# Performance work log

Measured on AMD Instinct MI355X. Metric: run time of the kernel, lower is better.

The kernel has to match this reference:

```python
import jax, jax.numpy as jnp
import numpy as np

THRESHOLD = 0.35      # overlap_thresh
NEGPOS_RATIO = 7
VAR0, VAR1 = 0.1, 0.2  # self.variance


def make_priors():
    # Standard RetinaFace 640x640 anchor grid -> 16800 priors (cx, cy, w, h)
    img = 640
    steps = [8, 16, 32]
    min_sizes = [[16, 32], [64, 128], [256, 512]]
    out = []
    for step, ms in zip(steps, min_sizes):
        f = img // step
        ii, jj = np.meshgrid(np.arange(f), np.arange(f), indexing="ij")
        cx = ((jj + 0.5) * step / img).ravel().astype(np.float32)
        cy = ((ii + 0.5) * step / img).ravel().astype(np.float32)
        for m in ms:
            s = np.full_like(cx, m / img)
            out.append(np.stack([cx, cy, s, s], axis=-1))
    return jnp.asarray(np.concatenate(out, axis=0), dtype=jnp.float32)


def jaccard(a, b):
    # a: [O,4] point-form gt boxes, b: [P,4] point-form priors -> IoU [O,P]
    lt = jnp.maximum(a[:, None, :2], b[None, :, :2])
    rb = jnp.minimum(a[:, None, 2:], b[None, :, 2:])
    wh = jnp.clip(rb - lt, 0.0)
    inter = wh[..., 0] * wh[..., 1]
    area_a = ((a[:, 2] - a[:, 0]) * (a[:, 3] - a[:, 1]))[:, None]
    area_b = ((b[:, 2] - b[:, 0]) * (b[:, 3] - b[:, 1]))[None, :]
    return inter / (area_a + area_b - inter)


def setup_inputs() -> dict:
    key = jax.random.key(0)
    ks = jax.random.split(key, 7)
    B, P, O = 64, 16800, 64
    loc_data = jax.random.normal(ks[0], (B, P, 4), jnp.float32)
    conf_data = jax.random.normal(ks[1], (B, P, 2), jnp.float32)
    landm_data = jax.random.normal(ks[2], (B, P, 10), jnp.float32)
    priors = make_priors()
    # targets: [B, O, 15] = [xmin ymin xmax ymax | 10 landmark coords | label]
    c = jax.random.uniform(ks[3], (B, O, 2), minval=0.15, maxval=0.85)
    wh = jax.random.uniform(ks[4], (B, O, 2), minval=0.05, maxval=0.3)
    boxes = jnp.concatenate([jnp.clip(c - wh / 2, 1e-3, 0.999),
                             jnp.clip(c + wh / 2, 1e-3, 0.999)], axis=-1)
    landms = jax.random.uniform(ks[5], (B, O, 10))
    lab = jnp.where(jax.random.uniform(ks[6], (B, O, 1)) < 0.8, 1.0, -1.0)
    targets = jnp.concatenate([boxes, landms, lab], axis=-1).astype(jnp.float32)
    return {"loc_data": loc_data, "conf_data": conf_data,
            "landm_data": landm_data, "priors": priors, "targets": targets}


def _smooth_l1(x):
    ax = jnp.abs(x)
    return jnp.where(ax < 1.0, 0.5 * ax * ax, ax - 0.5)


def reference(loc_data, conf_data, landm_data, priors, targets):
    B, P, C = conf_data.shape
    O = targets.shape[1]
    priors_pf = jnp.concatenate([priors[:, :2] - priors[:, 2:] * 0.5,
                                 priors[:, :2] + priors[:, 2:] * 0.5], axis=1)

    def match_one(t):
        truths = t[:, :4]
        landms = t[:, 4:14]
        labels = t[:, 14].astype(jnp.int32)
        ov = jaccard(truths, priors_pf)               # [O,P]
        bp_ov = ov.max(axis=1)                         # best prior per truth
        bp_idx = jnp.argmax(ov, axis=1)
        valid = bp_ov >= 0.2                           # RetinaFace gt filter
        bt_ov = ov.max(axis=0)                         # best truth per prior
        bt_idx = jnp.argmax(ov, axis=0)
        # index_fill_(best_prior_idx, 2) for valid gts, ensure best prior kept
        bt_ov = bt_ov.at[bp_idx].set(jnp.where(valid, 2.0, bt_ov[bp_idx]))
        bt_idx = bt_idx.at[bp_idx].set(jnp.arange(O))
        matched = truths[bt_idx]                       # [P,4] point form
        conf = labels[bt_idx]
        conf = jnp.where(bt_ov < THRESHOLD, 0, conf)
        # encode loc target
        g_cxcy = ((matched[:, :2] + matched[:, 2:]) * 0.5 - priors[:, :2]) / (VAR0 * priors[:, 2:])
        g_wh = jnp.log((matched[:, 2:] - matched[:, :2]) / priors[:, 2:]) / VAR1
        loc = jnp.concatenate([g_cxcy, g_wh], axis=1)
        # encode landmark target (5 points)
        ml = landms[bt_idx].reshape(P, 5, 2)
        lm = ((ml - priors[:, None, :2]) / (VAR0 * priors[:, None, 2:])).reshape(P, 10)
        any_valid = jnp.any(valid)                     # early-return branch of match()
        return (jnp.where(any_valid, loc, 0.0),
                jnp.where(any_valid, conf, 0),
                jnp.where(any_valid, lm, 0.0))

    loc_t, conf_t, landm_t = jax.vmap(match_one)(targets)
    loc_t = jax.lax.stop_gradient(loc_t)       # targets built from .data in torch
    landm_t = jax.lax.stop_gradient(landm_t)

    # landmark loss over conf_t > 0
    pos1 = conf_t > 0
    N1 = jnp.maximum(pos1.sum().astype(jnp.float32), 1.0)
    loss_landm = jnp.sum(jnp.where(pos1[..., None], _smooth_l1(landm_data - landm_t), 0.0))

    # localization loss over conf_t != 0 (labels -1 and 1 both positive)
    pos = conf_t != 0
    conf_t1 = jnp.where(pos, 1, conf_t)        # conf_t[pos] = 1 -> values in {0,1}
    loss_l = jnp.sum(jnp.where(pos[..., None], _smooth_l1(loc_data - loc_t), 0.0))

    # hard negative mining
    lse = jax.nn.logsumexp(conf_data, axis=2)                       # [B,P]
    picked = jnp.take_along_axis(conf_data, conf_t1[..., None], axis=2)[..., 0]
    ce_all = lse - picked                                            # per-anchor CE
    rank_score = jnp.where(pos, 0.0, ce_all)
    loss_idx = jnp.argsort(-rank_score, axis=1)
    idx_rank = jnp.argsort(loss_idx, axis=1)
    num_pos = pos.sum(axis=1, keepdims=True)
    num_neg = jnp.minimum(NEGPOS_RATIO * num_pos, P - 1)
    neg = idx_rank < num_neg
    union = pos | neg
    loss_c = jnp.sum(jnp.where(union, ce_all, 0.0))

    N = jnp.maximum(num_pos.sum().astype(jnp.float32), 1.0)
    return loss_l / N, loss_c / N, loss_landm / N1
```

## Files before the change

kernel.cpp:

```cpp
#include <hip/hip_runtime.h>
#include <math.h>

#define B 64
#define P 16800
#define O 64
#define THRESH 0.35f
#define VALID_T 0.2f
#define HB 2048
#define HSHIFT 21
#define AREA_M 0.34f
#define MULT 2
#define CHB (MULT * 256)
#define NB2 ((P + CHB - 1) / CHB)
#define KD1B (B * NB2)
#define KB2B (B * O / 4)

__device__ __forceinline__ float smooth_l1(float x) {
    float ax = fabsf(x);
    return ax < 1.f ? 0.5f * ax * ax : ax - 0.5f;
}
__device__ __forceinline__ float lse2(float c0, float c1) {
    float m = fmaxf(c0, c1);
    return m + __logf(__expf(c0 - m) + __expf(c1 - m));
}
__device__ __forceinline__ void iou_upd(float4 t, float area_a,
                                        float px1, float py1, float px2, float py2,
                                        float area_b,
                                        float& bnum, float& bden, int& bio, int o) {
    float w = fmaxf(fminf(t.z, px2) - fmaxf(t.x, px1), 0.f);
    float h = fmaxf(fminf(t.w, py2) - fmaxf(t.y, py1), 0.f);
    float inter = w * h;
    float den = area_a + area_b - inter;
    if (inter * bden > bnum * den) { bnum = inter; bden = den; bio = o; }
}
__device__ __forceinline__ float wave_sum(float v) {
#pragma unroll
    for (int s = 32; s > 0; s >>= 1) v += __shfl_down(v, s, 64);
    return v;
}
__device__ __forceinline__ int wave_sum_i(int v) {
#pragma unroll
    for (int s = 32; s > 0; s >>= 1) v += __shfl_down(v, s, 64);
    return v;
}
__device__ __forceinline__ float wave_min(float v) {
#pragma unroll
    for (int s = 32; s > 0; s >>= 1) v = fminf(v, __shfl_xor(v, s, 64));
    return v;
}
__device__ __forceinline__ float wave_max(float v) {
#pragma unroll
    for (int s = 32; s > 0; s >>= 1) v = fmaxf(v, __shfl_xor(v, s, 64));
    return v;
}
__device__ __forceinline__ int wave_sufscan(int v, int lane) {
#pragma unroll
    for (int s = 1; s < 64; s <<= 1) {
        int o = __shfl_down(v, s, 64);
        if (lane + s < 64) v += o;
    }
    return v;
}

__global__ void __launch_bounds__(256) kMain(
        const float* __restrict__ loc_data, const float* __restrict__ conf_data,
        const float* __restrict__ landm_data, const float* __restrict__ priors,
        const float* __restrict__ targets,
        float* __restrict__ rank,
        int* __restrict__ num_pos, float* __restrict__ pos_ce,
        float* __restrict__ gsum, int* __restrict__ np1_tot,
        unsigned long long* __restrict__ bp_final) {
    if (blockIdx.x >= KD1B) {
        int pair = (blockIdx.x - KD1B) * 4 + (threadIdx.x >> 6);
        int lane = threadIdx.x & 63;
        int o = pair & (O - 1);
        int b = pair >> 6;
        const float* tt = &targets[(b * O + o) * 15];
        float tx1 = tt[0], ty1 = tt[1], tx2 = tt[2], ty2 = tt[3];
        float area_a = (tx2 - tx1) * (ty2 - ty1);
        float4 tb = make_float4(tx1, ty1, tx2, ty2);
        float bn = 0.f, bd = 1.f;
        unsigned bp = 0u;
        const int fs[6]   = {80, 80, 40, 40, 20, 20};
        const int ms[6]   = {16, 32, 64, 128, 256, 512};
        const int base[6] = {0, 6400, 12800, 14400, 16000, 16400};
#pragma unroll
        for (int c = 0; c < 6; ++c) {
            int f = fs[c];
            float inv = (float)f;
            float h = (float)ms[c] * (0.5f / 640.f);
            int j0 = (int)floorf((tx1 - h) * inv - 0.5f) - 1; if (j0 < 0) j0 = 0;
            int j1 = (int)ceilf((tx2 + h) * inv - 0.5f) + 1;  if (j1 > f - 1) j1 = f - 1;
            int i0 = (int)floorf((ty1 - h) * inv - 0.5f) - 1; if (i0 < 0) i0 = 0;
            int i1 = (int)ceilf((ty2 + h) * inv - 0.5f) + 1;  if (i1 > f - 1) i1 = f - 1;
            if (j1 < j0 || i1 < i0) continue;
            int nj = j1 - j0 + 1;
            int n = (i1 - i0 + 1) * nj;
            float rcp_nj = 1.0f / (float)nj;
            for (int idx = lane; idx < n; idx += 64) {
                int ii = (int)((float)idx * rcp_nj);
                int jj = idx - ii * nj;
                if (jj < 0) { ii--; jj += nj; } else if (jj >= nj) { ii++; jj -= nj; }
                int p = base[c] + (i0 + ii) * f + (j0 + jj);
                float4 q = ((const float4*)priors)[p];
                float px1 = q.x - q.z * 0.5f, py1 = q.y - q.w * 0.5f;
                float px2 = q.x + q.z * 0.5f, py2 = q.y + q.w * 0.5f;
                float areab = (px2 - px1) * (py2 - py1);
                float w = fmaxf(fminf(tb.z, px2) - fmaxf(tb.x, px1), 0.f);
                float hh = fmaxf(fminf(tb.w, py2) - fmaxf(tb.y, py1), 0.f);
                float inter = w * hh;
                float den = area_a + areab - inter;
                float l = bn * den, r = inter * bd;
                if (r > l) { bn = inter; bd = den; bp = (unsigned)p; }
            }
        }
#pragma unroll
        for (int s = 32; s > 0; s >>= 1) {
            float no = __shfl_xor(bn, s, 64), dd = __shfl_xor(bd, s, 64);
            unsigned po = __shfl_xor(bp, s, 64);
            float l = bn * dd, r = no * bd;
            bool take = (r > l) || (r == l && po < bp);
            if (take) { bn = no; bd = dd; bp = po; }
        }
        if (lane == 0) {
            float iou = bn / bd;
            bp_final[b * O + o] = ((unsigned long long)__float_as_uint(iou) << 32)
                                | (unsigned)(0xFFFFFFFFu - bp);
        }
        return;
    }
    int blk = blockIdx.x % NB2;
    int b = blockIdx.x / NB2;
    int p0 = blk * CHB;
    __shared__ float4 t4[O];
    __shared__ float ta[O], lab[O];
    __shared__ float lm[O][10];
    __shared__ float4 wbb[4];
    __shared__ float2 wab[4];
    __shared__ int alist[O];
    __shared__ int s_cnt;
    __shared__ float wredf[3][4];
    __shared__ int wredi[2][4];
    int tid = threadIdx.x;
    if (tid < O) {
        const float* t = &targets[(b * O + tid) * 15];
        float a0 = t[0], a1 = t[1], a2 = t[2], a3 = t[3];
        t4[tid] = make_float4(a0, a1, a2, a3);
        ta[tid] = (a2 - a0) * (a3 - a1);
        lab[tid] = t[14];
    }
    for (int i = tid; i < O * 10; i += 256)
        lm[i / 10][i % 10] = targets[b * O * 15 + (i / 10) * 15 + 4 + (i % 10)];
    float px1[MULT], py1[MULT], px2[MULT], py2[MULT], areab[MULT];
    float4 pr4[MULT];
    float bnum[MULT], bden[MULT]; int bi[MULT]; bool act[MULT];
    float bx1 = 1e30f, by1 = 1e30f, bx2 = -1e30f, by2 = -1e30f;
    float amn = 1e30f, amx = -1e30f;
#pragma unroll
    for (int mi = 0; mi < MULT; ++mi) {
        int p = p0 + mi * 256 + tid;
        act[mi] = (p < P);
        int pc = act[mi] ? p : (P - 1);
        float4 q = ((const float4*)priors)[pc];
        pr4[mi] = q;
        px1[mi] = q.x - q.z * 0.5f; py1[mi] = q.y - q.w * 0.5f;
        px2[mi] = q.x + q.z * 0.5f; py2[mi] = q.y + q.w * 0.5f;
        areab[mi] = (px2[mi] - px1[mi]) * (py2[mi] - py1[mi]);
        bx1 = fminf(bx1, px1[mi]); by1 = fminf(by1, py1[mi]);
        bx2 = fmaxf(bx2, px2[mi]); by2 = fmaxf(by2, py2[mi]);
        amn = fminf(amn, areab[mi]); amx = fmaxf(amx, areab[mi]);
        bnum[mi] = 0.f; bden[mi] = 1.f; bi[mi] = 0;
    }
    bx1 = wave_min(bx1); by1 = wave_min(by1);
    bx2 = wave_max(bx2); by2 = wave_max(by2);
    amn = wave_min(amn); amx = wave_max(amx);
    int wid = tid >> 6, lid = tid & 63;
    if (lid == 0) { wbb[wid] = make_float4(bx1, by1, bx2, by2); wab[wid] = make_float2(amn, amx); }
    __syncthreads();
    if (tid < 64) {
        float ux1 = fminf(fminf(wbb[0].x, wbb[1].x), fminf(wbb[2].x, wbb[3].x));
        float uy1 = fminf(fminf(wbb[0].y, wbb[1].y), fminf(wbb[2].y, wbb[3].y));
        float ux2 = fmaxf(fmaxf(wbb[0].z, wbb[1].z), fmaxf(wbb[2].z, wbb[3].z));
        float uy2 = fmaxf(fmaxf(wbb[0].w, wbb[1].w), fmaxf(wbb[2].w, wbb[3].w));
        float bmn = fminf(fminf(wab[0].x, wab[1].x), fminf(wab[2].x, wab[3].x));
        float bmx = fmaxf(fmaxf(wab[0].y, wab[1].y), fmaxf(wab[2].y, wab[3].y));
        float4 t = t4[tid];
        float Aa = ta[tid];
        bool pass = (fminf(t.z, ux2) - fmaxf(t.x, ux1) > 0.f) &&
                    (fminf(t.w, uy2) - fmaxf(t.y, uy1) > 0.f) &&
                    (Aa >= AREA_M * bmn) && (bmx >= AREA_M * Aa);
        unsigned long long mask = __ballot(pass);
        if (tid == 0) s_cnt = __popcll(mask);
        if (pass) {
            int pos = __popcll(mask & ((1ull << tid) - 1ull));
            alist[pos] = tid;
        }
    }
    __syncthreads();
    int cnt = s_cnt;
    for (int li = 0; li < cnt; ++li) {
        int o = alist[li];
        float4 t = t4[o];
        float w0 = fminf(t.z, bx2) - fmaxf(t.x, bx1);
        float h0 = fminf(t.w, by2) - fmaxf(t.y, by1);
        if (w0 <= 0.f || h0 <= 0.f) continue;
        float Aa = ta[o];
#pragma unroll
        for (int mi = 0; mi < MULT; ++mi) {
            float Ap = areab[mi];
            if (Aa >= AREA_M * Ap && Ap >= AREA_M * Aa)
                iou_upd(t, Aa, px1[mi], py1[mi], px2[mi], py2[mi], Ap,
                        bnum[mi], bden[mi], bi[mi], o);
        }
    }
    float ll = 0.f, llm = 0.f, cep = 0.f;
    int cp = 0, cp1 = 0;
#pragma unroll
    for (int mi = 0; mi < MULT; ++mi) {
        if (!act[mi]) continue;
        int p = p0 + mi * 256 + tid;
        float best = bnum[mi] / bden[mi];
        int conf = (best >= THRESH) ? (int)lab[bi[mi]] : 0;
        float2 c01 = ((const float2*)conf_data)[b * P + p];
        float c0 = c01.x, c1 = c01.y;
        float lse = lse2(c0, c1);
        bool pos = conf != 0;
        float ce = lse - (pos ? c1 : c0);
        float rv = pos ? 0.f : ce;
        rank[(size_t)b * P + p] = rv;
        if (pos) {
            cp++; cep += ce;
            int ti = bi[mi];
            float cx = pr4[mi].x, cy = pr4[mi].y, sw = pr4[mi].z, sh = pr4[mi].w;
            float4 t = t4[ti];
            float gx = ((t.x + t.z) * 0.5f - cx) / (0.1f * sw);
            float gy = ((t.y + t.w) * 0.5f - cy) / (0.1f * sh);
            float gw = logf((t.z - t.x) / sw) / 0.2f;
            float gh = logf((t.w - t.y) / sh) / 0.2f;
            const float* ld = &loc_data[(size_t)(b * P + p) * 4];
            ll += smooth_l1(ld[0] - gx) + smooth_l1(ld[1] - gy) +
                  smooth_l1(ld[2] - gw) + smooth_l1(ld[3] - gh);
            if (conf > 0) {
                cp1++;
                const float* lmd = &landm_data[(size_t)(b * P + p) * 10];
                for (int k5 = 0; k5 < 5; ++k5) {
                    float lx = (lm[ti][k5 * 2 + 0] - cx) / (0.1f * sw);
                    float ly = (lm[ti][k5 * 2 + 1] - cy) / (0.1f * sh);
                    llm += smooth_l1(lmd[k5 * 2 + 0] - lx) + smooth_l1(lmd[k5 * 2 + 1] - ly);
                }
            }
        }
    }
    float s_ll = wave_sum(ll), s_llm = wave_sum(llm), s_cep = wave_sum(cep);
    int s_cp = wave_sum_i(cp), s_cp1 = wave_sum_i(cp1);
    if (lid == 0) {
        wredf[0][wid] = s_ll; wredf[1][wid] = s_llm; wredf[2][wid] = s_cep;
        wredi[0][wid] = s_cp; wredi[1][wid] = s_cp1;
    }
    __syncthreads();
    if (tid == 0) {
        float ll_t = wredf[0][0] + wredf[0][1] + wredf[0][2] + wredf[0][3];
        float llm_t = wredf[1][0] + wredf[1][1] + wredf[1][2] + wredf[1][3];
        float cep_t = wredf[2][0] + wredf[2][1] + wredf[2][2] + wredf[2][3];
        int cp_t = wredi[0][0] + wredi[0][1] + wredi[0][2] + wredi[0][3];
        int cp1_t = wredi[1][0] + wredi[1][1] + wredi[1][2] + wredi[1][3];
        if (ll_t != 0.f)  atomicAdd(&gsum[0], ll_t);
        if (llm_t != 0.f) atomicAdd(&gsum[1], llm_t);
        if (cep_t != 0.f) atomicAdd(&pos_ce[b], cep_t);
        if (cp_t)  atomicAdd(&num_pos[b], cp_t);
        if (cp1_t) atomicAdd(np1_tot, cp1_t);
    }
}

__global__ void __launch_bounds__(1024) kTail(
        const float* __restrict__ priors, const float* __restrict__ targets,
        const float* __restrict__ loc_data, const float* __restrict__ conf_data,
        const float* __restrict__ landm_data,
        const unsigned long long* __restrict__ bp_final,
        const float* __restrict__ rank,
        const int* __restrict__ num_pos, const float* __restrict__ pos_ce,
        float* __restrict__ gsum, int* __restrict__ np1_tot, int* __restrict__ np_tot,
        float* __restrict__ lossc_tot, int* __restrict__ done,
        float* __restrict__ out) {
    __shared__ __align__(16) unsigned lrow[P];
    __shared__ float4 t4[O];
    __shared__ float ta[O], lab[O];
    __shared__ int sp[O];
    __shared__ int lh[HB];
    __shared__ int chunkSum[256];
    __shared__ int suf[257];
    __shared__ int waveTot[4];
    __shared__ int hist2[256];
    __shared__ int s_np, s_bin0, s_kk0, s_bin, s_kk;
    __shared__ float wredf[16];
    __shared__ int wredi[16];
    __shared__ float s_sumgt;

    int b = blockIdx.x;
    int tid = threadIdx.x;
    const float* r = rank + (size_t)b * P;
    const float4* r4 = (const float4*)r;
    for (int i = tid; i < P / 4; i += 1024) {
        float4 q = r4[i];
        ((uint4*)lrow)[i] = make_uint4(__float_as_uint(q.x), __float_as_uint(q.y),
                                       __float_as_uint(q.z), __float_as_uint(q.w));
    }
    for (int i = tid; i < HB; i += 1024) lh[i] = 0;
    int p = 0, v = 0;
    if (tid < O) {
        const float* tt = &targets[(b * O + tid) * 15];
        float4 tj = make_float4(tt[0], tt[1], tt[2], tt[3]);
        t4[tid] = tj;
        ta[tid] = (tj.z - tj.x) * (tj.w - tj.y);
        lab[tid] = tt[14];
        unsigned long long kpk = bp_final[b * O + tid];
        p = (int)(0xFFFFFFFFu - (unsigned)(kpk & 0xFFFFFFFFu));
        float iou = __uint_as_float((unsigned)(kpk >> 32));
        v = (iou >= VALID_T) ? 1 : 0;
        sp[tid] = p;
    }
    __syncthreads();
    for (int i = tid; i < P; i += 1024) atomicAdd(&lh[lrow[i] >> HSHIFT], 1);
    __syncthreads();
    int dnp = 0, dn1 = 0;
    float dll = 0.f, dllm = 0.f, dce = 0.f;
    if (tid < O) {
        int j = tid;
        bool winner = true;
        for (int jj = j + 1; jj < O; ++jj)
            if (sp[jj] == p) { winner = false; break; }
        if (winner) {
            float4 q = ((const float4*)priors)[p];
            float px1 = q.x - q.z * 0.5f, py1 = q.y - q.w * 0.5f;
            float px2 = q.x + q.z * 0.5f, py2 = q.y + q.w * 0.5f;
            float areab = (px2 - px1) * (py2 - py1);
            float bnum = 0.f, bden = 1.f; int bi = 0;
            for (int o = 0; o < O; ++o) {
                float Aa = ta[o];
                if (Aa >= AREA_M * areab && areab >= AREA_M * Aa)
                    iou_upd(t4[o], Aa, px1, py1, px2, py2, areab, bnum, bden, bi, o);
            }
            float best = bnum / bden;
            float ov_new = v ? 2.0f : best;
            int conf_old = (best >= THRESH) ? (int)lab[bi] : 0;
            int conf_new = (ov_new >= THRESH) ? (int)lab[j] : 0;
            float2 c01 = ((const float2*)conf_data)[b * P + p];
            float c0 = c01.x, c1 = c01.y;
            float lse = lse2(c0, c1);
            bool po = conf_old != 0, pn = conf_new != 0;
            float ceo = lse - (po ? c1 : c0), cen = lse - (pn ? c1 : c0);
            float rvo = po ? 0.f : ceo, rvn = pn ? 0.f : cen;
            if (__float_as_uint(rvo) != __float_as_uint(rvn)) {
                lrow[p] = __float_as_uint(rvn);
                int bo = __float_as_uint(rvo) >> HSHIFT, bn = __float_as_uint(rvn) >> HSHIFT;
                if (bo != bn) { atomicAdd(&lh[bn], 1); atomicAdd(&lh[bo], -1); }
            }
            const float* ld = &loc_data[(size_t)(b * P + p) * 4];
            auto enc_ll = [&](int ti) -> float {
                float4 t = t4[ti];
                float gx = ((t.x + t.z) * 0.5f - q.x) / (0.1f * q.z);
                float gy = ((t.y + t.w) * 0.5f - q.y) / (0.1f * q.w);
                float gw = logf((t.z - t.x) / q.z) / 0.2f;
                float gh = logf((t.w - t.y) / q.w) / 0.2f;
                return smooth_l1(ld[0] - gx) + smooth_l1(ld[1] - gy) +
                       smooth_l1(ld[2] - gw) + smooth_l1(ld[3] - gh);
            };
            if (po) dll -= enc_ll(bi);
            if (pn) dll += enc_ll(j);
            dce = (pn ? cen : 0.f) - (po ? ceo : 0.f);
            dnp = (int)pn - (int)po;
            const float* lmd = &landm_data[(size_t)(b * P + p) * 10];
            auto enc_lm = [&](int ti) -> float {
                const float* lmt = &targets[(b * O + ti) * 15 + 4];
                float sum = 0.f;
                for (int k5 = 0; k5 < 5; ++k5) {
                    float lx = (lmt[k5 * 2 + 0] - q.x) / (0.1f * q.z);
                    float ly = (lmt[k5 * 2 + 1] - q.y) / (0.1f * q.w);
                    sum += smooth_l1(lmd[k5 * 2 + 0] - lx) + smooth_l1(lmd[k5 * 2 + 1] - ly);
                }
                return sum;
            };
            if (conf_old > 0) dllm -= enc_lm(bi);
            if (conf_new > 0) dllm += enc_lm(j);
            dn1 = (int)(conf_new > 0) - (int)(conf_old > 0);
        }
    }
    float pce_reg = 0.f;
    if (tid < 64) {
        float r_ll = wave_sum(dll), r_lm = wave_sum(dllm), r_ce = wave_sum(dce);
        int r_np = wave_sum_i(dnp), r_n1 = wave_sum_i(dn1);
        if (tid == 0) {
            if (r_ll != 0.f) atomicAdd(&gsum[0], r_ll);
            if (r_lm != 0.f) atomicAdd(&gsum[1], r_lm);
            pce_reg = pos_ce[b] + r_ce;
            int np = num_pos[b] + r_np;
            s_np = np;
            atomicAdd(np_tot, np);
            if (r_n1) atomicAdd(np1_tot, r_n1);
        }
    }
    __syncthreads();
    int k = s_np * 7;
    if (k > P - 1) k = P - 1;
    if (tid < 256) {
        int cs = 0;
#pragma unroll
        for (int i = 0; i < HB / 256; ++i) cs += lh[tid * (HB / 256) + i];
        chunkSum[tid] = cs;
    }
    if (tid == 0) { s_bin0 = (k <= 0) ? -1 : 0; s_kk0 = (k <= 0) ? 0 : k; }
    __syncthreads();
    {
        int lane = tid & 63;
        int vv = (tid < 256) ? chunkSum[tid] : 0;
        vv = wave_sufscan(vv, lane);
        if (tid < 256 && lane == 0) waveTot[tid >> 6] = vv;
        __syncthreads();
        if (tid < 256) {
            int after = 0;
            for (int g = (tid >> 6) + 1; g < 4; ++g) after += waveTot[g];
            suf[tid] = vv + after;
            if (tid == 0) suf[256] = 0;
        }
        __syncthreads();
        if (k > 0 && tid < 256) {
            if (suf[tid] >= k && suf[tid + 1] < k) {
                int cum = suf[tid + 1];
                for (int i = HB / 256 - 1; i >= 0; --i) {
                    int hv = lh[tid * (HB / 256) + i];
                    if (cum + hv >= k) { s_bin0 = tid * (HB / 256) + i; s_kk0 = k - cum; break; }
                    cum += hv;
                }
            }
        }
    }
    __syncthreads();
    int bin = s_bin0;
    int kk0 = s_kk0;
    float topk_b = 0.f;
    if (bin >= 0) {
        unsigned lo_bound = ((unsigned)(bin + 1)) << HSHIFT;
        float sumgt = 0.f;
        for (int pp = tid; pp < P; pp += 1024) {
            unsigned u = lrow[pp];
            if (u >= lo_bound) sumgt += __uint_as_float(u);
        }
        float sg = wave_sum(sumgt);
        if ((tid & 63) == 0) wredf[tid >> 6] = sg;
        __syncthreads();
        if (tid == 0) {
            float t = 0.f;
            for (int i = 0; i < 16; ++i) t += wredf[i];
            s_sumgt = t;
        }
        unsigned pref = ((unsigned)bin) << HSHIFT;
        unsigned resolved = 0xFFFFFFFFu << HSHIFT;
        int kk = kk0;
        const int shifts[3] = {13, 5, 0};
        const int nbins[3] = {256, 256, 32};
        for (int pass = 0; pass < 3; ++pass) {
            int sh = shifts[pass], nb = nbins[pass];
            if (tid < nb) hist2[tid] = 0;
            __syncthreads();
            for (int i = tid; i < P / 4; i += 1024) {
                uint4 u4 = ((const uint4*)lrow)[i];
                if ((u4.x & resolved) == pref) atomicAdd(&hist2[(u4.x >> sh) & (nb - 1)], 1);
                if ((u4.y & resolved) == pref) atomicAdd(&hist2[(u4.y >> sh) & (nb - 1)], 1);
                if ((u4.z & resolved) == pref) atomicAdd(&hist2[(u4.z >> sh) & (nb - 1)], 1);
                if ((u4.w & resolved) == pref) atomicAdd(&hist2[(u4.w >> sh) & (nb - 1)], 1);
            }
            __syncthreads();
            int lane = tid & 63;
            int vv = (tid < nb) ? hist2[tid] : 0;
            vv = wave_sufscan(vv, lane);
            if (tid < nb && lane == 0) waveTot[tid >> 6] = vv;
            __syncthreads();
            int ng = (nb + 63) >> 6;
            if (tid < nb) {
                int after = 0;
                for (int g = (tid >> 6) + 1; g < ng; ++g) after += waveTot[g];
                suf[tid] = vv + after;
                if (tid == 0) suf[nb] = 0;
            }
            __syncthreads();
            if (tid < nb) {
                if (suf[tid] >= kk && suf[tid + 1] < kk) { s_bin = tid; s_kk = kk - suf[tid + 1]; }
            }
            __syncthreads();
            pref |= ((unsigned)s_bin) << sh;
            resolved |= (unsigned)(nb - 1) << sh;
            kk = s_kk;
            __syncthreads();
        }
        float tv = __uint_as_float(pref);
        float sumS = 0.f; int cntS = 0;
        for (int pp = tid; pp < P; pp += 1024) {
            unsigned u = lrow[pp];
            if ((u >> HSHIFT) == (unsigned)bin) {
                float val = __uint_as_float(u);
                if (val > tv) { sumS += val; cntS++; }
            }
        }
        float s2 = wave_sum(sumS); int c2 = wave_sum_i(cntS);
        if ((tid & 63) == 0) { wredf[tid >> 6] = s2; wredi[tid >> 6] = c2; }
        __syncthreads();
        if (tid == 0) {
            float st = 0.f; int ct = 0;
            for (int i = 0; i < 16; ++i) { st += wredf[i]; ct += wredi[i]; }
            topk_b = s_sumgt + st + (float)(kk0 - ct) * tv;
        }
    }
    if (tid == 0) {
        atomicAdd(lossc_tot, pce_reg + topk_b);
        __threadfence();
        int old = atomicAdd(done, 1);
        if (old == B - 1) {
            float g0 = atomicAdd(&gsum[0], 0.f);
            float g1 = atomicAdd(&gsum[1], 0.f);
            float lc = atomicAdd(lossc_tot, 0.f);
            int np = atomicAdd(np_tot, 0);
            int n1 = atomicAdd(np1_tot, 0);
            float N = fmaxf((float)np, 1.f);
            float N1 = fmaxf((float)n1, 1.f);
            out[0] = g0 / N;
            out[1] = lc / N;
            out[2] = g1 / N1;
        }
    }
}

extern "C" void kernel_launch(void* const* d_in, const int* in_sizes, int n_in,
                              void* d_out, int out_size, void* d_ws, size_t ws_size,
                              hipStream_t stream) {
    const float* loc_data   = (const float*)d_in[0];
    const float* conf_data  = (const float*)d_in[1];
    const float* landm_data = (const float*)d_in[2];
    const float* priors     = (const float*)d_in[3];
    const float* targets    = (const float*)d_in[4];
    float* out = (float*)d_out;

    char* ws = (char*)d_ws;
    size_t off = 0;
    auto alloc = [&](size_t bytes) -> void* {
        void* pp = ws + off;
        off += (bytes + 255) & ~(size_t)255;
        return pp;
    };
    float* rank     = (float*)alloc((size_t)B * P * 4);
    unsigned long long* bp_final = (unsigned long long*)alloc((size_t)B * O * 8);
    size_t acc_bytes = (size_t)(2 * B * 4 + 64);
    char* acc = (char*)alloc(acc_bytes);
    int*   num_pos      = (int*)acc;
    float* pos_ce       = (float*)(acc + B * 4);
    float* gsum         = (float*)(acc + 2 * B * 4);
    int*   np1_tot      = (int*)(acc + 2 * B * 4 + 8);
    int*   np_tot       = (int*)(acc + 2 * B * 4 + 12);
    float* lossc_tot    = (float*)(acc + 2 * B * 4 + 16);
    int*   done         = (int*)(acc + 2 * B * 4 + 20);

    hipMemsetAsync(acc, 0, acc_bytes, stream);
    kMain<<<dim3(KD1B + KB2B), dim3(256), 0, stream>>>(loc_data, conf_data, landm_data,
                                                       priors, targets, rank,
                                                       num_pos, pos_ce, gsum, np1_tot,
                                                       bp_final);
    kTail<<<dim3(B), dim3(1024), 0, stream>>>(priors, targets, loc_data, conf_data,
                                              landm_data, bp_final, rank,
                                              num_pos, pos_ce, gsum, np1_tot, np_tot,
                                              lossc_tot, done, out);
}
```

Measured before the change: 166.8 us.

## Compact radix-select candidates into shared memory and fuse histogram with row load

The per-batch top-k radix select now builds the first histogram while copying the rank row into shared memory. During the tail-sum pass it compacts values from the boundary bin into a shared candidate list (capped at CCAP) and builds the second-level histogram in the same pass, so later refinement passes scan only the candidates instead of the full row. The first kernel doubles MULT to 4 priors per thread and stages the raw targets with one float4 copy into shared memory. These changes add shared memory use and a fallback path when the candidate list overflows.

Result: slower. 170.9 us (+2.4%).

```diff
diff --git a/kernel.cpp b/kernel.cpp
--- a/kernel.cpp
+++ b/kernel.cpp
@@ -9,7 +9,8 @@
 #define HB 2048
 #define HSHIFT 21
 #define AREA_M 0.34f
-#define MULT 2
+#define CCAP 4096
+#define MULT 4
 #define CHB (MULT * 256)
 #define NB2 ((P + CHB - 1) / CHB)
 #define KD1B (B * NB2)
@@ -132,9 +133,9 @@
     int blk = blockIdx.x % NB2;
     int b = blockIdx.x / NB2;
     int p0 = blk * CHB;
+    __shared__ float traw[O * 15];
     __shared__ float4 t4[O];
     __shared__ float ta[O], lab[O];
-    __shared__ float lm[O][10];
     __shared__ float4 wbb[4];
     __shared__ float2 wab[4];
     __shared__ int alist[O];
@@ -142,15 +143,8 @@
     __shared__ float wredf[3][4];
     __shared__ int wredi[2][4];
     int tid = threadIdx.x;
-    if (tid < O) {
-        const float* t = &targets[(b * O + tid) * 15];
-        float a0 = t[0], a1 = t[1], a2 = t[2], a3 = t[3];
-        t4[tid] = make_float4(a0, a1, a2, a3);
-        ta[tid] = (a2 - a0) * (a3 - a1);
-        lab[tid] = t[14];
-    }
-    for (int i = tid; i < O * 10; i += 256)
-        lm[i / 10][i % 10] = targets[b * O * 15 + (i / 10) * 15 + 4 + (i % 10)];
+    if (tid < O * 15 / 4)
+        ((float4*)traw)[tid] = ((const float4*)(targets + (size_t)b * O * 15))[tid];
     float px1[MULT], py1[MULT], px2[MULT], py2[MULT], areab[MULT];
     float4 pr4[MULT];
     float bnum[MULT], bden[MULT]; int bi[MULT]; bool act[MULT];
@@ -178,14 +172,19 @@
     if (lid == 0) { wbb[wid] = make_float4(bx1, by1, bx2, by2); wab[wid] = make_float2(amn, amx); }
     __syncthreads();
     if (tid < 64) {
+        const float* tr = &traw[tid * 15];
+        float a0 = tr[0], a1 = tr[1], a2 = tr[2], a3 = tr[3];
+        float4 t = make_float4(a0, a1, a2, a3);
+        t4[tid] = t;
+        float Aa = (a2 - a0) * (a3 - a1);
+        ta[tid] = Aa;
+        lab[tid] = tr[14];
         float ux1 = fminf(fminf(wbb[0].x, wbb[1].x), fminf(wbb[2].x, wbb[3].x));
         float uy1 = fminf(fminf(wbb[0].y, wbb[1].y), fminf(wbb[2].y, wbb[3].y));
         float ux2 = fmaxf(fmaxf(wbb[0].z, wbb[1].z), fmaxf(wbb[2].z, wbb[3].z));
         float uy2 = fmaxf(fmaxf(wbb[0].w, wbb[1].w), fmaxf(wbb[2].w, wbb[3].w));
         float bmn = fminf(fminf(wab[0].x, wab[1].x), fminf(wab[2].x, wab[3].x));
         float bmx = fmaxf(fmaxf(wab[0].y, wab[1].y), fmaxf(wab[2].y, wab[3].y));
-        float4 t = t4[tid];
-        float Aa = ta[tid];
         bool pass = (fminf(t.z, ux2) - fmaxf(t.x, ux1) > 0.f) &&
                     (fminf(t.w, uy2) - fmaxf(t.y, uy1) > 0.f) &&
                     (Aa >= AREA_M * bmn) && (bmx >= AREA_M * Aa);
@@ -243,9 +242,10 @@
             if (conf > 0) {
                 cp1++;
                 const float* lmd = &landm_data[(size_t)(b * P + p) * 10];
+                const float* lmt = &traw[ti * 15 + 4];
                 for (int k5 = 0; k5 < 5; ++k5) {
-                    float lx = (lm[ti][k5 * 2 + 0] - cx) / (0.1f * sw);
-                    float ly = (lm[ti][k5 * 2 + 1] - cy) / (0.1f * sh);
+                    float lx = (lmt[k5 * 2 + 0] - cx) / (0.1f * sw);
+                    float ly = (lmt[k5 * 2 + 1] - cy) / (0.1f * sh);
                     llm += smooth_l1(lmd[k5 * 2 + 0] - lx) + smooth_l1(lmd[k5 * 2 + 1] - ly);
                 }
             }
@@ -291,7 +291,8 @@
     __shared__ int suf[257];
     __shared__ int waveTot[4];
     __shared__ int hist2[256];
-    __shared__ int s_np, s_bin0, s_kk0, s_bin, s_kk;
+    __shared__ unsigned lcand[CCAP];
+    __shared__ int s_np, s_bin0, s_kk0, s_bin, s_kk, s_cnt;
     __shared__ float wredf[16];
     __shared__ int wredi[16];
     __shared__ float s_sumgt;
@@ -299,13 +300,8 @@
     int b = blockIdx.x;
     int tid = threadIdx.x;
     const float* r = rank + (size_t)b * P;
-    const float4* r4 = (const float4*)r;
-    for (int i = tid; i < P / 4; i += 1024) {
-        float4 q = r4[i];
-        ((uint4*)lrow)[i] = make_uint4(__float_as_uint(q.x), __float_as_uint(q.y),
-                                       __float_as_uint(q.z), __float_as_uint(q.w));
-    }
     for (int i = tid; i < HB; i += 1024) lh[i] = 0;
+    if (tid == 0) s_cnt = 0;
     int p = 0, v = 0;
     if (tid < O) {
         const float* tt = &targets[(b * O + tid) * 15];
@@ -320,7 +316,17 @@
         sp[tid] = p;
     }
     __syncthreads();
-    for (int i = tid; i < P; i += 1024) atomicAdd(&lh[lrow[i] >> HSHIFT], 1);
+    const float4* r4 = (const float4*)r;
+    for (int i = tid; i < P / 4; i += 1024) {
+        float4 q = r4[i];
+        uint4 u = make_uint4(__float_as_uint(q.x), __float_as_uint(q.y),
+                             __float_as_uint(q.z), __float_as_uint(q.w));
+        ((uint4*)lrow)[i] = u;
+        atomicAdd(&lh[u.x >> HSHIFT], 1);
+        atomicAdd(&lh[u.y >> HSHIFT], 1);
+        atomicAdd(&lh[u.z >> HSHIFT], 1);
+        atomicAdd(&lh[u.w >> HSHIFT], 1);
+    }
     __syncthreads();
     int dnp = 0, dn1 = 0;
     float dll = 0.f, dllm = 0.f, dce = 0.f;
@@ -439,11 +445,19 @@
     int kk0 = s_kk0;
     float topk_b = 0.f;
     if (bin >= 0) {
+        if (tid < 256) hist2[tid] = 0;
+        __syncthreads();
         unsigned lo_bound = ((unsigned)(bin + 1)) << HSHIFT;
         float sumgt = 0.f;
-        for (int pp = tid; pp < P; pp += 1024) {
-            unsigned u = lrow[pp];
-            if (u >= lo_bound) sumgt += __uint_as_float(u);
+        for (int i = tid; i < P / 4; i += 1024) {
+            uint4 u4 = ((const uint4*)lrow)[i];
+#define TAIL_H(u) { if ((u) >= lo_bound) sumgt += __uint_as_float(u); \
+                    else if (((u) >> HSHIFT) == (unsigned)bin) { \
+                        int idx = atomicAdd(&s_cnt, 1); \
+                        if (idx < CCAP) lcand[idx] = (u); \
+                        atomicAdd(&hist2[((u) >> 13) & 255], 1); } }
+            TAIL_H(u4.x) TAIL_H(u4.y) TAIL_H(u4.z) TAIL_H(u4.w)
+#undef TAIL_H
         }
         float sg = wave_sum(sumgt);
         if ((tid & 63) == 0) wredf[tid >> 6] = sg;
@@ -453,40 +467,65 @@
             for (int i = 0; i < 16; ++i) t += wredf[i];
             s_sumgt = t;
         }
-        unsigned pref = ((unsigned)bin) << HSHIFT;
-        unsigned resolved = 0xFFFFFFFFu << HSHIFT;
-        int kk = kk0;
-        const int shifts[3] = {13, 5, 0};
-        const int nbins[3] = {256, 256, 32};
-        for (int pass = 0; pass < 3; ++pass) {
-            int sh = shifts[pass], nb = nbins[pass];
-            if (tid < nb) hist2[tid] = 0;
-            __syncthreads();
-            for (int i = tid; i < P / 4; i += 1024) {
-                uint4 u4 = ((const uint4*)lrow)[i];
-                if ((u4.x & resolved) == pref) atomicAdd(&hist2[(u4.x >> sh) & (nb - 1)], 1);
-                if ((u4.y & resolved) == pref) atomicAdd(&hist2[(u4.y >> sh) & (nb - 1)], 1);
-                if ((u4.z & resolved) == pref) atomicAdd(&hist2[(u4.z >> sh) & (nb - 1)], 1);
-                if ((u4.w & resolved) == pref) atomicAdd(&hist2[(u4.w >> sh) & (nb - 1)], 1);
-            }
-            __syncthreads();
-            int lane = tid & 63;
+        {
+            int lane = tid & 63, nb = 256;
             int vv = (tid < nb) ? hist2[tid] : 0;
             vv = wave_sufscan(vv, lane);
             if (tid < nb && lane == 0) waveTot[tid >> 6] = vv;
             __syncthreads();
-            int ng = (nb + 63) >> 6;
             if (tid < nb) {
                 int after = 0;
-                for (int g = (tid >> 6) + 1; g < ng; ++g) after += waveTot[g];
+                for (int g = (tid >> 6) + 1; g < 4; ++g) after += waveTot[g];
                 suf[tid] = vv + after;
                 if (tid == 0) suf[nb] = 0;
             }
             __syncthreads();
             if (tid < nb) {
-                if (suf[tid] >= kk && suf[tid + 1] < kk) { s_bin = tid; s_kk = kk - suf[tid + 1]; }
+                if (suf[tid] >= kk0 && suf[tid + 1] < kk0) { s_bin = tid; s_kk = kk0 - suf[tid + 1]; }
             }
             __syncthreads();
+        }
+        unsigned pref = (((unsigned)bin) << HSHIFT) | (((unsigned)s_bin) << 13);
+        unsigned resolved = (0xFFFFFFFFu << HSHIFT) | (255u << 13);
+        int kk = s_kk;
+        int m = s_cnt;
+        bool useG = (m > CCAP);
+        for (int pass = 0; pass < 2; ++pass) {
+            int sh = pass == 0 ? 5 : 0;
+            int nb = pass == 0 ? 256 : 32;
+            if (tid < nb) hist2[tid] = 0;
+            __syncthreads();
+            if (!useG) {
+                for (int i = tid; i < m; i += 1024) {
+                    unsigned u = lcand[i];
+                    if ((u & resolved) == pref) atomicAdd(&hist2[(u >> sh) & (nb - 1)], 1);
+                }
+            } else {
+                for (int pp = tid; pp < P; pp += 1024) {
+                    unsigned u = lrow[pp];
+                    if ((u & resolved) == pref) atomicAdd(&hist2[(u >> sh) & (nb - 1)], 1);
+                }
+            }
+            __syncthreads();
+            {
+                int lane = tid & 63;
+                int vv = (tid < nb) ? hist2[tid] : 0;
+                vv = wave_sufscan(vv, lane);
+                if (tid < nb && lane == 0) waveTot[tid >> 6] = vv;
+                __syncthreads();
+                int ng = (nb + 63) >> 6;
+                if (tid < nb) {
+                    int after = 0;
+                    for (int g = (tid >> 6) + 1; g < ng; ++g) after += waveTot[g];
+                    suf[tid] = vv + after;
+                    if (tid == 0) suf[nb] = 0;
+                }
+                __syncthreads();
+                if (tid < nb) {
+                    if (suf[tid] >= kk && suf[tid + 1] < kk) { s_bin = tid; s_kk = kk - suf[tid + 1]; }
+                }
+                __syncthreads();
+            }
             pref |= ((unsigned)s_bin) << sh;
             resolved |= (unsigned)(nb - 1) << sh;
             kk = s_kk;
```
